# Optimization experiments

Hardware: AMD Instinct MI355X
Metric: run time of the kernel (lower is better)

## Reference

```python
import jax, jax.numpy as jnp
import numpy as np

# Table config matching init_kwargs: 8 mixed-dim tables, 250k rows each.
TABLE_ROWS = [250000] * 8
TABLE_DIMS = [16, 32, 64, 128, 16, 32, 64, 128]
T = len(TABLE_DIMS)
B = 8192          # batch size
L = 32            # fixed bag (pooling) length; offsets = arange(T*B+1)*L
TOTAL_W = sum(r * d for r, d in zip(TABLE_ROWS, TABLE_DIMS))  # 120,000,000
NNZ = T * B * L   # 2,097,152 total lookups


def setup_inputs() -> dict:
    key = jax.random.key(0)
    k_w, k_i, k_p = jax.random.split(key, 3)
    weights = jax.random.normal(k_w, (TOTAL_W,), dtype=jnp.float32)
    indices = jax.random.randint(k_i, (NNZ,), 0, TABLE_ROWS[0], dtype=jnp.int64)
    offsets = (jnp.arange(T * B + 1, dtype=jnp.int64) * L)
    per_sample_weights = jax.random.uniform(k_p, (NNZ,), dtype=jnp.float32)
    return {"weights": weights, "indices": indices, "offsets": offsets,
            "per_sample_weights": per_sample_weights}


def reference(weights, indices, offsets, per_sample_weights):
    # Table-major layout: indices/per_sample_weights are [T, B, L] flattened,
    # bags are fixed length L (encoded by the uniform-stride `offsets`).
    idx = indices.reshape(T, B, L)
    psw = per_sample_weights.reshape(T, B, L)
    outs = []
    w_off = 0
    for t in range(T):
        r, d = TABLE_ROWS[t], TABLE_DIMS[t]
        Wt = jax.lax.dynamic_slice(weights, (w_off,), (r * d,)).reshape(r, d)
        emb = Wt[idx[t]]                                  # [B, L, d] gather
        outs.append(jnp.einsum('bld,bl->bd', emb, psw[t]))  # weighted-sum pool
        w_off += r * d
    return jnp.concatenate(outs, axis=1)                  # [B, total_D]
```

## Files before the change

### kernel.cpp

```cpp
#include <hip/hip_runtime.h>
#include <hip/hip_bf16.h>


#define T_TABLES 8
#define BATCH    8192
#define BAG_L    32
#define GROUPS_PER_ROW 120
#define TOTAL_GROUPS (BATCH * GROUPS_PER_ROW)

__constant__ int   c_bound[9] = {0, 4, 12, 28, 60, 64, 72, 88, 120};
__constant__ int   c_dim[8]   = {16, 32, 64, 128, 16, 32, 64, 128};
__constant__ unsigned c_woff[8] = {0u, 4000000u, 12000000u, 28000000u,
                                   60000000u, 64000000u, 72000000u, 88000000u};

__global__ __launch_bounds__(256) void emb_bags_kernel(
    const float* __restrict__ weights,
    const int*   __restrict__ indices,
    const float* __restrict__ psw,
    float*       __restrict__ out)
{
    const int g = blockIdx.x * blockDim.x + threadIdx.x;
    const int b = g / GROUPS_PER_ROW;
    const int c = g - b * GROUPS_PER_ROW;

    const int t = (c >= 4) + (c >= 12) + (c >= 28) + (c >= 60)
                + (c >= 64) + (c >= 72) + (c >= 88);

    const int      dim   = c_dim[t];
    const unsigned wbase = c_woff[t] + (unsigned)(c - c_bound[t]) * 4u;
    const int      ibase = (t * BATCH + b) * BAG_L;

    const int*   idx = indices + ibase;
    const float* pw  = psw + ibase;

    float4 acc = make_float4(0.f, 0.f, 0.f, 0.f);
#pragma unroll 8
    for (int l = 0; l < BAG_L; ++l) {
        const unsigned row = (unsigned)idx[l];
        const float    w   = pw[l];
        const float4 v = *(const float4*)(weights + (size_t)(wbase + row * (unsigned)dim));
        acc.x += v.x * w;
        acc.y += v.y * w;
        acc.z += v.z * w;
        acc.w += v.w * w;
    }
    ((float4*)out)[g] = acc;
}

extern "C" void kernel_launch(void* const* d_in, const int* in_sizes, int n_in,
                              void* d_out, int out_size, void* d_ws, size_t ws_size,
                              hipStream_t stream) {
    const float* weights = (const float*)d_in[0];
    const int*   indices = (const int*)d_in[1];
    const float* psw     = (const float*)d_in[3];
    float*       out     = (float*)d_out;

    const int block = 256;
    const int grid  = TOTAL_GROUPS / block;
    emb_bags_kernel<<<grid, block, 0, stream>>>(weights, indices, psw, out);
}
```

Baseline: 611.1 us.

## Remap groups table-major with grid-stride loop and vectorized index loads

Reorders the thread-to-work mapping so consecutive threads process the same table and batch row, using power-of-two shifts instead of division. Switches to a persistent grid-stride launch with fixed 1024 blocks and loads indices and per-sample weights as int4/float4. Intended to improve coalescing and reduce index-fetch and address overhead, at the cost of scattered output writes and possibly lower memory-level parallelism from the smaller grid.

```diff
diff --git a/kernel.cpp b/kernel.cpp
--- a/kernel.cpp
+++ b/kernel.cpp
@@ -1,50 +1,68 @@
 #include <hip/hip_runtime.h>
-#include <hip/hip_bf16.h>
 
 
-#define T_TABLES 8
 #define BATCH    8192
 #define BAG_L    32
 #define GROUPS_PER_ROW 120
 #define TOTAL_GROUPS (BATCH * GROUPS_PER_ROW)
+#define NBLOCKS  1024
+#define NTHREADS 256
+#define GRID_THREADS (NBLOCKS * NTHREADS)
 
-__constant__ int   c_bound[9] = {0, 4, 12, 28, 60, 64, 72, 88, 120};
-__constant__ int   c_dim[8]   = {16, 32, 64, 128, 16, 32, 64, 128};
+__constant__ unsigned c_pref[8] = {0u, 32768u, 98304u, 229376u,
+                                   491520u, 524288u, 589824u, 720896u};
+__constant__ int      c_s[8]    = {2, 3, 4, 5, 2, 3, 4, 5};
+__constant__ int      c_cb[8]   = {0, 4, 12, 28, 60, 64, 72, 88};
 __constant__ unsigned c_woff[8] = {0u, 4000000u, 12000000u, 28000000u,
                                    60000000u, 64000000u, 72000000u, 88000000u};
 
-__global__ __launch_bounds__(256) void emb_bags_kernel(
+__global__ __launch_bounds__(NTHREADS, 4) void emb_bags_kernel(
     const float* __restrict__ weights,
     const int*   __restrict__ indices,
     const float* __restrict__ psw,
     float*       __restrict__ out)
 {
-    const int g = blockIdx.x * blockDim.x + threadIdx.x;
-    const int b = g / GROUPS_PER_ROW;
-    const int c = g - b * GROUPS_PER_ROW;
+    const unsigned tid = blockIdx.x * NTHREADS + threadIdx.x;
 
-    const int t = (c >= 4) + (c >= 12) + (c >= 28) + (c >= 60)
-                + (c >= 64) + (c >= 72) + (c >= 88);
+    for (unsigned g = tid; g < TOTAL_GROUPS; g += GRID_THREADS) {
+        const int t = (g >= 32768u) + (g >= 98304u) + (g >= 229376u)
+                    + (g >= 491520u) + (g >= 524288u) + (g >= 589824u)
+                    + (g >= 720896u);
 
-    const int      dim   = c_dim[t];
-    const unsigned wbase = c_woff[t] + (unsigned)(c - c_bound[t]) * 4u;
-    const int      ibase = (t * BATCH + b) * BAG_L;
+        const int      s     = c_s[t];
+        const unsigned local = g - c_pref[t];
+        const unsigned b     = local >> s;
+        const unsigned cg    = local & ((1u << s) - 1u);
+        const int      ld    = s + 2;
+        const unsigned wbase = c_woff[t] + (cg << 2);
 
-    const int*   idx = indices + ibase;
-    const float* pw  = psw + ibase;
+        const unsigned ibase = ((unsigned)(t * BATCH) + b) << 5;
+        const int4*   idx4 = (const int4*)(indices + ibase);
+        const float4* pw4  = (const float4*)(psw + ibase);
 
-    float4 acc = make_float4(0.f, 0.f, 0.f, 0.f);
-#pragma unroll 8
-    for (int l = 0; l < BAG_L; ++l) {
-        const unsigned row = (unsigned)idx[l];
-        const float    w   = pw[l];
-        const float4 v = *(const float4*)(weights + (size_t)(wbase + row * (unsigned)dim));
-        acc.x += v.x * w;
-        acc.y += v.y * w;
-        acc.z += v.z * w;
-        acc.w += v.w * w;
+        float4 acc = make_float4(0.f, 0.f, 0.f, 0.f);
+#pragma unroll 2
+        for (int j = 0; j < 8; ++j) {
+            const int4   i4 = idx4[j];
+            const float4 w4 = pw4[j];
+
+            const float4 v0 = *(const float4*)(weights + (size_t)(wbase + ((unsigned)i4.x << ld)));
+            const float4 v1 = *(const float4*)(weights + (size_t)(wbase + ((unsigned)i4.y << ld)));
+            const float4 v2 = *(const float4*)(weights + (size_t)(wbase + ((unsigned)i4.z << ld)));
+            const float4 v3 = *(const float4*)(weights + (size_t)(wbase + ((unsigned)i4.w << ld)));
+
+            acc.x += v0.x * w4.x; acc.y += v0.y * w4.x;
+            acc.z += v0.z * w4.x; acc.w += v0.w * w4.x;
+            acc.x += v1.x * w4.y; acc.y += v1.y * w4.y;
+            acc.z += v1.z * w4.y; acc.w += v1.w * w4.y;
+            acc.x += v2.x * w4.z; acc.y += v2.y * w4.z;
+            acc.z += v2.z * w4.z; acc.w += v2.w * w4.z;
+            acc.x += v3.x * w4.w; acc.y += v3.y * w4.w;
+            acc.z += v3.z * w4.w; acc.w += v3.w * w4.w;
+        }
+
+        ((float4*)out)[b * GROUPS_PER_ROW + c_cb[t] + cg] = acc;
     }
-    ((float4*)out)[g] = acc;
 }
 
 extern "C" void kernel_launch(void* const* d_in, const int* in_sizes, int n_in,
@@ -55,7 +73,5 @@
     const float* psw     = (const float*)d_in[3];
     float*       out     = (float*)d_out;
 
-    const int block = 256;
-    const int grid  = TOTAL_GROUPS / block;
-    emb_bags_kernel<<<grid, block, 0, stream>>>(weights, indices, psw, out);
+    emb_bags_kernel<<<NBLOCKS, NTHREADS, 0, stream>>>(weights, indices, psw, out);
 }
```

New measurement: 603.7 us. No clear change (-1.2%).
